# Kernel tuning notes

Hardware: AMD Instinct MI355X
Metric: run time of the kernel (lower is better)

## Reference

```python
import jax, jax.numpy as jnp
import numpy as np
import math

B, S, DIM, H, HD = 2, 2048, 2048, 16, 128


def _rotary(t, cos, sin):
    # t: [B, S, H, HD]; cos/sin: [S, HD//2]
    tr = t.reshape(*t.shape[:-1], HD // 2, 2)
    t_re, t_im = tr[..., 0], tr[..., 1]
    c = cos[None, :, None, :]
    s = sin[None, :, None, :]
    o_re = t_re * c - t_im * s
    o_im = t_re * s + t_im * c
    out = jnp.stack([o_re, o_im], axis=-1)
    return out.reshape(t.shape)


def setup_inputs() -> dict:
    key = jax.random.key(0)
    ks = jax.random.split(key, 6)
    x = jax.random.normal(ks[0], (B, S, DIM), dtype=jnp.float32)
    # rotary frequencies (base 10000), matching complex freqs_cis = exp(i * t * freq)
    inv_freq = 1.0 / (10000.0 ** (np.arange(0, HD, 2, dtype=np.float32) / HD))
    t = np.arange(S, dtype=np.float32)
    ang = np.outer(t, inv_freq)  # [S, HD//2]
    freqs_cos = jnp.asarray(np.cos(ang), dtype=jnp.float32)
    freqs_sin = jnp.asarray(np.sin(ang), dtype=jnp.float32)
    # causal boolean mask [1,1,S,S]
    mask = jnp.tril(jnp.ones((S, S), dtype=bool))[None, None]
    scale = 0.02
    qw = jax.random.normal(ks[1], (DIM, H * HD), dtype=jnp.float32) * scale
    kw = jax.random.normal(ks[2], (DIM, H * HD), dtype=jnp.float32) * scale
    vw = jax.random.normal(ks[3], (DIM, H * HD), dtype=jnp.float32) * scale
    ow = jax.random.normal(ks[4], (H * HD, DIM), dtype=jnp.float32) * scale
    return {"x": x, "freqs_cos": freqs_cos, "freqs_sin": freqs_sin, "mask": mask,
            "qw": qw, "kw": kw, "vw": vw, "ow": ow}


def reference(x, freqs_cos, freqs_sin, mask, qw, kw, vw, ow):
    bsz, slen, _ = x.shape
    q = (x @ qw).reshape(bsz, slen, H, HD)
    k = (x @ kw).reshape(bsz, slen, H, HD)
    v = (x @ vw).reshape(bsz, slen, H, HD)
    q = _rotary(q, freqs_cos[:slen], freqs_sin[:slen])
    k = _rotary(k, freqs_cos[:slen], freqs_sin[:slen])
    # [B, H, S, HD]
    q = q.transpose(0, 2, 1, 3)
    k = k.transpose(0, 2, 1, 3)
    v = v.transpose(0, 2, 1, 3)
    scale = 1.0 / math.sqrt(HD)
    scores = jnp.einsum('bhqd,bhkd->bhqk', q, k) * scale
    neg_inf = jnp.finfo(scores.dtype).min
    scores = jnp.where(mask, scores, neg_inf)
    attn_w = jax.nn.softmax(scores, axis=-1)
    attn = jnp.einsum('bhqk,bhkd->bhqd', attn_w, v)
    attn = attn.transpose(0, 2, 1, 3).reshape(bsz, slen, H * HD)
    out = attn @ ow
    return (out, attn_w)
```

## Files before the change

### kernel.cpp

```cpp
#include <hip/hip_runtime.h>
#include <stdint.h>

#define S 2048
#define DIMM 2048
#define NH 16
#define HD 128
#define NB 2
#define M4 4096

typedef unsigned short u16;
typedef unsigned int u32;
typedef __attribute__((ext_vector_type(8))) short short8;
typedef __attribute__((ext_vector_type(4))) float f32x4;

__device__ __forceinline__ u16 f2bf(float f) {
  union { float f; u32 u; } v; v.f = f;
  u32 u = v.u + 0x7fffu + ((v.u >> 16) & 1u);
  return (u16)(u >> 16);
}
__device__ __forceinline__ float bf2f(u16 b) {
  union { u32 u; float f; } v; v.u = ((u32)b) << 16;
  return v.f;
}
__device__ __forceinline__ u32 cvt_pk_bf16(float lo, float hi) {
  u32 r; asm("v_cvt_pk_bf16_f32 %0, %1, %2" : "=v"(r) : "v"(lo), "v"(hi)); return r;
}
__device__ __forceinline__ void gl_lds16(const void* g, void* l) {
  __builtin_amdgcn_global_load_lds((const __attribute__((address_space(1))) void*)g,
                                   (__attribute__((address_space(3))) void*)l, 16, 0, 0);
}
#define MFMA16(a, b, c) __builtin_amdgcn_mfma_f32_16x16x32_bf16(a, b, c, 0, 0, 0)

__global__ __launch_bounds__(256) void k_conv_x(const float* __restrict__ x, u16* __restrict__ xb) {
  int i = (blockIdx.x * 256 + threadIdx.x) * 8;
  float4 a = *(const float4*)&x[i];
  float4 b = *(const float4*)&x[i + 4];
  uint4 o;
  o.x = (u32)f2bf(a.x) | ((u32)f2bf(a.y) << 16);
  o.y = (u32)f2bf(a.z) | ((u32)f2bf(a.w) << 16);
  o.z = (u32)f2bf(b.x) | ((u32)f2bf(b.y) << 16);
  o.w = (u32)f2bf(b.z) | ((u32)f2bf(b.w) << 16);
  *(uint4*)&xb[i] = o;
}

__global__ __launch_bounds__(256) void k_transpose_w4(const float* __restrict__ w0, const float* __restrict__ w1,
                                                      const float* __restrict__ w2, const float* __restrict__ w3,
                                                      u16* __restrict__ t0, u16* __restrict__ t1,
                                                      u16* __restrict__ t2, u16* __restrict__ t3) {
  __shared__ u16 t[64][72];
  int zi = blockIdx.z;
  const float* w = (zi == 0) ? w0 : (zi == 1) ? w1 : (zi == 2) ? w2 : w3;
  u16* wt = (zi == 0) ? t0 : (zi == 1) ? t1 : (zi == 2) ? t2 : t3;
  int k0 = blockIdx.y * 64, n0 = blockIdx.x * 64;
  int tid = threadIdx.x;
  int r0 = tid >> 4, c4 = (tid & 15) * 4;
#pragma unroll
  for (int p = 0; p < 4; ++p) {
    int r = r0 + p * 16;
    float4 v = *(const float4*)&w[(size_t)(k0 + r) * DIMM + n0 + c4];
    t[c4 + 0][r] = f2bf(v.x); t[c4 + 1][r] = f2bf(v.y);
    t[c4 + 2][r] = f2bf(v.z); t[c4 + 3][r] = f2bf(v.w);
  }
  __syncthreads();
#pragma unroll
  for (int p = 0; p < 2; ++p) {
    int cc = tid + p * 256;
    int rn = cc >> 3, ck = (cc & 7) * 8;
    *(uint4*)&wt[(size_t)(n0 + rn) * DIMM + k0 + ck] = *(const uint4*)&t[rn][ck];
  }
}

__device__ __forceinline__ void gemm128_core(const u16* __restrict__ A, const u16* __restrict__ Bt,
                                             int m0, int n0, int Kd, u16* lA, u16* lB,
                                             f32x4 acc[4][4]) {
  int tid = threadIdx.x;
  int lane = tid & 63;
  int wid = tid >> 6;
  int wm = wid >> 1, wn = wid & 1;
  int c0 = tid, c1 = tid + 256;
  int a_r0 = c0 >> 2, a_k0 = (c0 & 3) * 8;
  int a_r1 = c1 >> 2, a_k1 = (c1 & 3) * 8;
  int ln = lane & 15, sub = lane >> 4;
  for (int kt = 0; kt < Kd; kt += 32) {
    gl_lds16(&A[(size_t)(m0 + a_r0) * Kd + kt + a_k0], &lA[c0 * 8]);
    gl_lds16(&A[(size_t)(m0 + a_r1) * Kd + kt + a_k1], &lA[c1 * 8]);
    gl_lds16(&Bt[(size_t)(n0 + a_r0) * Kd + kt + a_k0], &lB[c0 * 8]);
    gl_lds16(&Bt[(size_t)(n0 + a_r1) * Kd + kt + a_k1], &lB[c1 * 8]);
    __syncthreads();
    short8 af[4], bf[4];
#pragma unroll
    for (int mf = 0; mf < 4; ++mf)
      af[mf] = *(const short8*)&lA[(wm * 64 + mf * 16 + ln) * 32 + sub * 8];
#pragma unroll
    for (int nf = 0; nf < 4; ++nf)
      bf[nf] = *(const short8*)&lB[(wn * 64 + nf * 16 + ln) * 32 + sub * 8];
#pragma unroll
    for (int mf = 0; mf < 4; ++mf)
#pragma unroll
      for (int nf = 0; nf < 4; ++nf)
        acc[mf][nf] = MFMA16(af[mf], bf[nf], acc[mf][nf]);
    __syncthreads();
  }
}

__global__ __launch_bounds__(256) void k_gemm_qkv(const u16* __restrict__ xb,
                                                  const u16* __restrict__ qwT, const u16* __restrict__ kwT,
                                                  const u16* __restrict__ vwT,
                                                  const float* __restrict__ fc, const float* __restrict__ fs,
                                                  u16* __restrict__ qws, u16* __restrict__ kws,
                                                  u16* __restrict__ vtws) {
  __shared__ u16 lA[128 * 32], lB[128 * 32];
  int f = blockIdx.y * 48 + blockIdx.x;
  int fp = (f & 7) * 192 + (f >> 3);
  int bx = fp % 48, byy = fp / 48;

  int region = bx >> 4;
  const u16* Bt = (region == 0) ? qwT : ((region == 1) ? kwT : vwT);
  int n0 = (bx & 15) * 128;
  int m0 = byy * 128;
  f32x4 acc[4][4];
  f32x4 z4 = {0.f, 0.f, 0.f, 0.f};
#pragma unroll
  for (int i = 0; i < 4; ++i)
#pragma unroll
    for (int j = 0; j < 4; ++j) acc[i][j] = z4;
  gemm128_core(xb, Bt, m0, n0, DIMM, lA, lB, acc);
  int lane = threadIdx.x & 63, wid = threadIdx.x >> 6;
  int wm = wid >> 1, wn = wid & 1;
  int ln = lane & 15, sub = lane >> 4;
  if (region == 2) {
#pragma unroll
    for (int mf = 0; mf < 4; ++mf)
#pragma unroll
      for (int nf = 0; nf < 4; ++nf) {
        int m = m0 + wm * 64 + mf * 16 + sub * 4;
        int nl = n0 + wn * 64 + nf * 16 + ln;
        int b = m >> 11, s = m & 2047;
        int h = nl >> 7, d = nl & 127;
        u32 w0 = cvt_pk_bf16(acc[mf][nf][0], acc[mf][nf][1]);
        u32 w1 = cvt_pk_bf16(acc[mf][nf][2], acc[mf][nf][3]);
        uint2 pw = {w0, w1};
        *(uint2*)&vtws[((size_t)((b << 4) + h) * HD + d) * S + s] = pw;
      }
  } else {
    u16* dst = (region == 0) ? qws : kws;
#pragma unroll
    for (int mf = 0; mf < 4; ++mf)
#pragma unroll
      for (int nf = 0; nf < 4; ++nf) {
        int mbase = m0 + wm * 64 + mf * 16 + sub * 4;
        int nl = n0 + wn * 64 + nf * 16 + ln;
        int h = nl >> 7, d = nl & 127;
        int pi = d >> 1;
#pragma unroll
        for (int r = 0; r < 4; ++r) {
          int m = mbase + r;
          int b = m >> 11, s = m & 2047;
          float c = fc[s * 64 + pi];
          float sn = fs[s * 64 + pi];
          float v = acc[mf][nf][r];
          float prt = __shfl_xor(v, 1);
          float o = (ln & 1) ? (prt * sn + v * c) : (v * c - prt * sn);
          float o2 = __shfl_xor(o, 1);
          if (!(ln & 1)) {
            u32 opk = cvt_pk_bf16(o, o2);
            *(u32*)&dst[((size_t)((b << 4) + h) * S + s) * HD + d] = opk;
          }
        }
      }
  }
}

__global__ __launch_bounds__(256, 4) void k_attn(const u16* __restrict__ qws, const u16* __restrict__ kws,
                                                 const u16* __restrict__ vtws,
                                                 float* __restrict__ aw_all, u16* __restrict__ att) {
  __shared__ u16 lK[2][32 * 128];
  __shared__ u16 lV[2][128 * 32];
  __shared__ u16 lP[64 * 32];

  int f = blockIdx.x;
  int x = f & 7;
  int j = f >> 3;
  int cu = j & 31;
  int u = j >> 5;
  int by = 4 * x + u;
  int c2 = (u & 2) ? ((cu + 16) & 31) : cu;
  int qt = (u & 1) ? (31 - c2) : c2;
  int b = by >> 4, h = by & 15;
  const u16* qb = qws + (size_t)by * S * HD;
  const u16* kb = kws + (size_t)by * S * HD;
  const u16* vb = vtws + (size_t)by * HD * S;
  float* aw = aw_all + (size_t)by * S * S;
  int tid = threadIdx.x, lane = tid & 63, w = tid >> 6;
  int sub = lane >> 4, ln = lane & 15;
  int l7 = ln & 7, l3 = ln & 3;
  int q0 = qt * 64;
  int qrow = w * 16 + ln;
  int nkt = 2 * qt + 2;
  const float SC = 0.08838834764831845f * 1.4426950408889634f;

  auto stageK = [&](int kt, int bs) {
#pragma unroll
    for (int i = 0; i < 2; ++i) {
      int c = tid + i * 256;
      int row = c >> 4, p = c & 15;
      gl_lds16(&kb[(size_t)(kt * 32 + row) * HD + ((p ^ (row & 7)) << 3)], &lK[bs][c * 8]);
    }
  };
  auto stageV = [&](int kt, int bs) {
#pragma unroll
    for (int i = 0; i < 2; ++i) {
      int c = tid + i * 256;
      int row = c >> 2, p = c & 3;
      gl_lds16(&vb[(size_t)row * S + kt * 32 + ((p ^ (row & 3)) << 3)], &lV[bs][c * 8]);
    }
  };

  u16* lVlin = &lV[0][0];
#pragma unroll
  for (int i = 0; i < 4; ++i) {
    int c = tid + i * 256;
    int row = c >> 4, p = c & 15;
    gl_lds16(&qb[(size_t)(q0 + row) * HD + ((p ^ (row & 7)) << 3)], &lVlin[c * 8]);
  }
  stageK(0, 0);
  __syncthreads();

  short8 qf[4];
#pragma unroll
  for (int ks = 0; ks < 4; ++ks)
    qf[ks] = *(const short8*)&lVlin[qrow * 128 + (((ks * 4 + sub) ^ l7) << 3)];

  float ts = 0.f;
  for (int kt = 0; kt < nkt; ++kt) {
    int cur = kt & 1;
    if (kt + 1 < nkt) stageK(kt + 1, cur ^ 1);
    f32x4 sacc[2];
#pragma unroll
    for (int nf = 0; nf < 2; ++nf) sacc[nf] = f32x4{0.f, 0.f, 0.f, 0.f};
    __builtin_amdgcn_s_setprio(1);
#pragma unroll
    for (int nf = 0; nf < 2; ++nf) {
      int krow = nf * 16 + ln;
#pragma unroll
      for (int ks = 0; ks < 4; ++ks) {
        short8 kf = *(const short8*)&lK[cur][krow * 128 + (((ks * 4 + sub) ^ l7) << 3)];
        sacc[nf] = MFMA16(kf, qf[ks], sacc[nf]);
      }
    }
    __builtin_amdgcn_s_setprio(0);
    bool msk = (kt >= 2 * qt);
#pragma unroll
    for (int nf = 0; nf < 2; ++nf)
#pragma unroll
      for (int r = 0; r < 4; ++r) {
        float zz = sacc[nf][r] * SC;
        bool dead = msk && (kt * 32 + nf * 16 + sub * 4 + r > q0 + qrow);
        if (!dead) ts += exp2f(zz);
      }
    __syncthreads();
  }
  ts += __shfl_xor(ts, 16);
  ts += __shfl_xor(ts, 32);
  float mb = __log2f(ts);

  f32x4 oacc[8];
#pragma unroll
  for (int i = 0; i < 8; ++i) oacc[i] = f32x4{0.f, 0.f, 0.f, 0.f};
  stageK(nkt - 1, 0);
  stageV(nkt - 1, 0);
  __syncthreads();
  for (int it = 0; it < nkt; ++it) {
    int kt = nkt - 1 - it;
    int cur = it & 1;
    if (it + 1 < nkt) { stageK(kt - 1, cur ^ 1); stageV(kt - 1, cur ^ 1); }
    f32x4 sacc[2];
#pragma unroll
    for (int nf = 0; nf < 2; ++nf) sacc[nf] = f32x4{0.f, 0.f, 0.f, 0.f};
    __builtin_amdgcn_s_setprio(1);
#pragma unroll
    for (int nf = 0; nf < 2; ++nf) {
      int krow = nf * 16 + ln;
#pragma unroll
      for (int ks = 0; ks < 4; ++ks) {
        short8 kf = *(const short8*)&lK[cur][krow * 128 + (((ks * 4 + sub) ^ l7) << 3)];
        sacc[nf] = MFMA16(kf, qf[ks], sacc[nf]);
      }
    }
    __builtin_amdgcn_s_setprio(0);
    bool msk = (kt >= 2 * qt);
#pragma unroll
    for (int nf = 0; nf < 2; ++nf) {
      float p0 = exp2f(sacc[nf][0] * SC - mb);
      float p1 = exp2f(sacc[nf][1] * SC - mb);
      float p2 = exp2f(sacc[nf][2] * SC - mb);
      float p3 = exp2f(sacc[nf][3] * SC - mb);
      if (msk) {
        int base = kt * 32 + nf * 16 + sub * 4 - (q0 + qrow);
        if (base + 0 > 0) p0 = 0.f;
        if (base + 1 > 0) p1 = 0.f;
        if (base + 2 > 0) p2 = 0.f;
        if (base + 3 > 0) p3 = 0.f;
      }
      f32x4 pv = {p0, p1, p2, p3};
      __builtin_nontemporal_store(pv, (f32x4*)&aw[(size_t)(q0 + qrow) * S + kt * 32 + nf * 16 + sub * 4]);
      u32 w0 = cvt_pk_bf16(p0, p1);
      u32 w1 = cvt_pk_bf16(p2, p3);
      uint2 pw = {w0, w1};
      int c16 = (2 * nf + (sub >> 1)) ^ l3;
      *(uint2*)&lP[qrow * 32 + (c16 << 3) + ((sub & 1) << 2)] = pw;
    }
    short8 pa = *(const short8*)&lP[qrow * 32 + ((sub ^ l3) << 3)];
    __builtin_amdgcn_s_setprio(1);
#pragma unroll
    for (int nf2 = 0; nf2 < 8; ++nf2) {
      int drow = nf2 * 16 + ln;
      short8 vv = *(const short8*)&lV[cur][drow * 32 + ((sub ^ (drow & 3)) << 3)];
      oacc[nf2] = MFMA16(vv, pa, oacc[nf2]);
    }
    __builtin_amdgcn_s_setprio(0);
    __syncthreads();
  }

#pragma unroll
  for (int nf2 = 0; nf2 < 8; ++nf2) {
    u32 w0 = cvt_pk_bf16(oacc[nf2][0], oacc[nf2][1]);
    u32 w1 = cvt_pk_bf16(oacc[nf2][2], oacc[nf2][3]);
    uint2 ow2 = {w0, w1};
    *(uint2*)&att[(size_t)(b * S + q0 + qrow) * (NH * HD) + h * 128 + nf2 * 16 + sub * 4] = ow2;
  }

  {
    f32x4 zf = {0.f, 0.f, 0.f, 0.f};
    for (int kt2 = qt + 1; kt2 < 32; ++kt2) {
      float* base = aw + (size_t)q0 * S + kt2 * 64;
#pragma unroll
      for (int i = 0; i < 4; ++i) {
        int c = i * 256 + tid;
        int row = c >> 4, col = (c & 15) * 4;
        __builtin_nontemporal_store(zf, (f32x4*)&base[(size_t)row * S + col]);
      }
    }
  }
}

__global__ __launch_bounds__(256) void k_gemm_out(const u16* __restrict__ att, const u16* __restrict__ owT,
                                                  float* __restrict__ out) {
  __shared__ u16 lA[128 * 32], lB[128 * 32];
  int f = blockIdx.y * 16 + blockIdx.x;
  int fp = (f & 7) * 64 + (f >> 3);
  int n0 = (fp & 15) * 128, m0 = (fp >> 4) * 128;
  f32x4 acc[4][4];
  f32x4 z4 = {0.f, 0.f, 0.f, 0.f};
#pragma unroll
  for (int i = 0; i < 4; ++i)
#pragma unroll
    for (int j = 0; j < 4; ++j) acc[i][j] = z4;
  gemm128_core(att, owT, m0, n0, DIMM, lA, lB, acc);
  int lane = threadIdx.x & 63, wid = threadIdx.x >> 6;
  int wm = wid >> 1, wn = wid & 1;
  int ln = lane & 15, sub = lane >> 4;
#pragma unroll
  for (int mf = 0; mf < 4; ++mf)
#pragma unroll
    for (int nf = 0; nf < 4; ++nf)
#pragma unroll
      for (int r = 0; r < 4; ++r) {
        int m = m0 + wm * 64 + mf * 16 + sub * 4 + r;
        int nl = n0 + wn * 64 + nf * 16 + ln;
        out[(size_t)m * DIMM + nl] = acc[mf][nf][r];
      }
}

extern "C" void kernel_launch(void* const* d_in, const int* in_sizes, int n_in,
                              void* d_out, int out_size, void* d_ws, size_t ws_size,
                              hipStream_t stream) {
  const float* x  = (const float*)d_in[0];
  const float* fc = (const float*)d_in[1];
  const float* fs = (const float*)d_in[2];
  const float* qw = (const float*)d_in[4];
  const float* kw = (const float*)d_in[5];
  const float* vw = (const float*)d_in[6];
  const float* ow = (const float*)d_in[7];
  float* out = (float*)d_out;
  float* aw  = out + (size_t)M4 * DIMM;

  char* wsb = (char*)d_ws;
  u16* xb   = (u16*)(wsb);
  u16* qwT  = (u16*)(wsb + (size_t)16 * 1024 * 1024);
  u16* kwT  = (u16*)(wsb + (size_t)24 * 1024 * 1024);
  u16* vwT  = (u16*)(wsb + (size_t)32 * 1024 * 1024);
  u16* owT  = (u16*)(wsb + (size_t)40 * 1024 * 1024);
  u16* qws  = (u16*)(wsb + (size_t)48 * 1024 * 1024);
  u16* kws  = (u16*)(wsb + (size_t)64 * 1024 * 1024);
  u16* vtws = (u16*)(wsb + (size_t)80 * 1024 * 1024);
  u16* att  = (u16*)(wsb + (size_t)96 * 1024 * 1024);

  k_conv_x<<<4096, 256, 0, stream>>>(x, xb);
  k_transpose_w4<<<dim3(32, 32, 4), 256, 0, stream>>>(qw, kw, vw, ow, qwT, kwT, vwT, owT);
  k_gemm_qkv<<<dim3(48, 32), 256, 0, stream>>>(xb, qwT, kwT, vwT, fc, fs, qws, kws, vtws);
  k_attn<<<1024, 256, 0, stream>>>(qws, kws, vtws, aw, att);
  k_gemm_out<<<dim3(16, 32), 256, 0, stream>>>(att, owT, out);
}
```

Before: 383.3 us.

## Read K fragments directly from global memory and merge prep kernels

```diff
diff --git a/kernel.cpp b/kernel.cpp
--- a/kernel.cpp
+++ b/kernel.cpp
@@ -31,28 +31,30 @@
 }
 #define MFMA16(a, b, c) __builtin_amdgcn_mfma_f32_16x16x32_bf16(a, b, c, 0, 0, 0)
 
-__global__ __launch_bounds__(256) void k_conv_x(const float* __restrict__ x, u16* __restrict__ xb) {
-  int i = (blockIdx.x * 256 + threadIdx.x) * 8;
-  float4 a = *(const float4*)&x[i];
-  float4 b = *(const float4*)&x[i + 4];
-  uint4 o;
-  o.x = (u32)f2bf(a.x) | ((u32)f2bf(a.y) << 16);
-  o.y = (u32)f2bf(a.z) | ((u32)f2bf(a.w) << 16);
-  o.z = (u32)f2bf(b.x) | ((u32)f2bf(b.y) << 16);
-  o.w = (u32)f2bf(b.z) | ((u32)f2bf(b.w) << 16);
-  *(uint4*)&xb[i] = o;
-}
-
-__global__ __launch_bounds__(256) void k_transpose_w4(const float* __restrict__ w0, const float* __restrict__ w1,
-                                                      const float* __restrict__ w2, const float* __restrict__ w3,
-                                                      u16* __restrict__ t0, u16* __restrict__ t1,
-                                                      u16* __restrict__ t2, u16* __restrict__ t3) {
+__global__ __launch_bounds__(256) void k_prep(const float* __restrict__ x, u16* __restrict__ xb,
+                                              const float* __restrict__ w0, const float* __restrict__ w1,
+                                              const float* __restrict__ w2, const float* __restrict__ w3,
+                                              u16* __restrict__ t0, u16* __restrict__ t1,
+                                              u16* __restrict__ t2, u16* __restrict__ t3) {
+  int zi = blockIdx.z;
+  int tid = threadIdx.x;
+  if (zi >= 4) {
+    int bid = (zi - 4) * 1024 + blockIdx.y * 32 + blockIdx.x;
+    int i = (bid * 256 + tid) * 8;
+    float4 a = *(const float4*)&x[i];
+    float4 b = *(const float4*)&x[i + 4];
+    uint4 o;
+    o.x = (u32)f2bf(a.x) | ((u32)f2bf(a.y) << 16);
+    o.y = (u32)f2bf(a.z) | ((u32)f2bf(a.w) << 16);
+    o.z = (u32)f2bf(b.x) | ((u32)f2bf(b.y) << 16);
+    o.w = (u32)f2bf(b.z) | ((u32)f2bf(b.w) << 16);
+    *(uint4*)&xb[i] = o;
+    return;
+  }
   __shared__ u16 t[64][72];
-  int zi = blockIdx.z;
   const float* w = (zi == 0) ? w0 : (zi == 1) ? w1 : (zi == 2) ? w2 : w3;
   u16* wt = (zi == 0) ? t0 : (zi == 1) ? t1 : (zi == 2) ? t2 : t3;
   int k0 = blockIdx.y * 64, n0 = blockIdx.x * 64;
-  int tid = threadIdx.x;
   int r0 = tid >> 4, c4 = (tid & 15) * 4;
 #pragma unroll
   for (int p = 0; p < 4; ++p) {
@@ -174,7 +176,6 @@
 __global__ __launch_bounds__(256, 4) void k_attn(const u16* __restrict__ qws, const u16* __restrict__ kws,
                                                  const u16* __restrict__ vtws,
                                                  float* __restrict__ aw_all, u16* __restrict__ att) {
-  __shared__ u16 lK[2][32 * 128];
   __shared__ u16 lV[2][128 * 32];
   __shared__ u16 lP[64 * 32];
 
@@ -199,14 +200,6 @@
   int nkt = 2 * qt + 2;
   const float SC = 0.08838834764831845f * 1.4426950408889634f;
 
-  auto stageK = [&](int kt, int bs) {
-#pragma unroll
-    for (int i = 0; i < 2; ++i) {
-      int c = tid + i * 256;
-      int row = c >> 4, p = c & 15;
-      gl_lds16(&kb[(size_t)(kt * 32 + row) * HD + ((p ^ (row & 7)) << 3)], &lK[bs][c * 8]);
-    }
-  };
   auto stageV = [&](int kt, int bs) {
 #pragma unroll
     for (int i = 0; i < 2; ++i) {
@@ -223,7 +216,6 @@
     int row = c >> 4, p = c & 15;
     gl_lds16(&qb[(size_t)(q0 + row) * HD + ((p ^ (row & 7)) << 3)], &lVlin[c * 8]);
   }
-  stageK(0, 0);
   __syncthreads();
 
   short8 qf[4];
@@ -233,22 +225,19 @@
 
   float ts = 0.f;
   for (int kt = 0; kt < nkt; ++kt) {
-    int cur = kt & 1;
-    if (kt + 1 < nkt) stageK(kt + 1, cur ^ 1);
+    const u16* kbase = kb + (size_t)(kt * 32) * HD;
     f32x4 sacc[2];
 #pragma unroll
     for (int nf = 0; nf < 2; ++nf) sacc[nf] = f32x4{0.f, 0.f, 0.f, 0.f};
-    __builtin_amdgcn_s_setprio(1);
 #pragma unroll
     for (int nf = 0; nf < 2; ++nf) {
-      int krow = nf * 16 + ln;
+      const u16* rp = kbase + (size_t)(nf * 16 + ln) * HD;
 #pragma unroll
       for (int ks = 0; ks < 4; ++ks) {
-        short8 kf = *(const short8*)&lK[cur][krow * 128 + (((ks * 4 + sub) ^ l7) << 3)];
+        short8 kf = *(const short8*)&rp[(ks * 4 + sub) * 8];
         sacc[nf] = MFMA16(kf, qf[ks], sacc[nf]);
       }
     }
-    __builtin_amdgcn_s_setprio(0);
     bool msk = (kt >= 2 * qt);
 #pragma unroll
     for (int nf = 0; nf < 2; ++nf)
@@ -258,7 +247,6 @@
         bool dead = msk && (kt * 32 + nf * 16 + sub * 4 + r > q0 + qrow);
         if (!dead) ts += exp2f(zz);
       }
-    __syncthreads();
   }
   ts += __shfl_xor(ts, 16);
   ts += __shfl_xor(ts, 32);
@@ -267,23 +255,24 @@
   f32x4 oacc[8];
 #pragma unroll
   for (int i = 0; i < 8; ++i) oacc[i] = f32x4{0.f, 0.f, 0.f, 0.f};
-  stageK(nkt - 1, 0);
+  __syncthreads();
   stageV(nkt - 1, 0);
   __syncthreads();
   for (int it = 0; it < nkt; ++it) {
     int kt = nkt - 1 - it;
     int cur = it & 1;
-    if (it + 1 < nkt) { stageK(kt - 1, cur ^ 1); stageV(kt - 1, cur ^ 1); }
+    if (it + 1 < nkt) stageV(kt - 1, cur ^ 1);
+    const u16* kbase = kb + (size_t)(kt * 32) * HD;
     f32x4 sacc[2];
 #pragma unroll
     for (int nf = 0; nf < 2; ++nf) sacc[nf] = f32x4{0.f, 0.f, 0.f, 0.f};
     __builtin_amdgcn_s_setprio(1);
 #pragma unroll
     for (int nf = 0; nf < 2; ++nf) {
-      int krow = nf * 16 + ln;
+      const u16* rp = kbase + (size_t)(nf * 16 + ln) * HD;
 #pragma unroll
       for (int ks = 0; ks < 4; ++ks) {
-        short8 kf = *(const short8*)&lK[cur][krow * 128 + (((ks * 4 + sub) ^ l7) << 3)];
+        short8 kf = *(const short8*)&rp[(ks * 4 + sub) * 8];
         sacc[nf] = MFMA16(kf, qf[ks], sacc[nf]);
       }
     }
@@ -396,8 +385,7 @@
   u16* vtws = (u16*)(wsb + (size_t)80 * 1024 * 1024);
   u16* att  = (u16*)(wsb + (size_t)96 * 1024 * 1024);
 
-  k_conv_x<<<4096, 256, 0, stream>>>(x, xb);
-  k_transpose_w4<<<dim3(32, 32, 4), 256, 0, stream>>>(qw, kw, vw, ow, qwT, kwT, vwT, owT);
+  k_prep<<<dim3(32, 32, 8), 256, 0, stream>>>(x, xb, qw, kw, vw, ow, qwT, kwT, vwT, owT);
   k_gemm_qkv<<<dim3(48, 32), 256, 0, stream>>>(xb, qwT, kwT, vwT, fc, fs, qws, kws, vtws);
   k_attn<<<1024, 256, 0, stream>>>(qws, kws, vtws, aw, att);
   k_gemm_out<<<dim3(16, 32), 256, 0, stream>>>(att, owT, out);
```

Measured after the change: 497.3 us. +29.7%, slower.
